# Kernel optimization log

Hardware: AMD Instinct MI355X
Metric: run time of the kernel (lower is better)

## Reference

```python
import math
import jax, jax.numpy as jnp
from jax import lax
import numpy as np

B, HH, WW = 8, 128, 128
N = HH * WW
DIM, NH = 256, 4
HD = DIM // 2 // NH          # 32, per-head dim of the halved channels
CH = DIM // 2                # 128
THETA, MAXSEQ = 10000.0, 4096

# --- static FoPE frequency setup (mirrors RotaryEmbedding.get_inv_freq with fope=True) ---
def _inv_freq():
    rot = 2 * HD                                   # rotary dim = d_model//n_heads = 2*head_dim
    inv = 1.0 / THETA ** (np.arange(0, rot, 2, dtype=np.float64) / rot)
    return inv[inv >= 2.0 * np.pi / MAXSEQ].astype(np.float32)

INV_FREQ = _inv_freq()
D_IN = int(INV_FREQ.shape[0])                      # 23
D_OUT = D_IN if D_IN <= (2 * HD) // 4 else (2 * HD) // 4   # 16


def _coef(key, gain=0.5):
    # xavier_normal_ on (NH, D_IN, D_OUT) + step-eye offset, as in FourierEmbedding.__init__
    fan_in, fan_out = D_IN * D_OUT, NH * D_OUT
    std = gain * math.sqrt(2.0 / (fan_in + fan_out))
    c = std * jax.random.normal(key, (NH, D_IN, D_OUT), jnp.float32)
    step = math.ceil(D_IN / D_OUT)
    eye = np.zeros((NH, D_IN, D_OUT), np.float32)
    for i in range(D_OUT):
        if i * step < D_IN:
            eye[:, i * step, i] = 1.0
    return c + jnp.asarray(eye)


def setup_inputs() -> dict:
    key = jax.random.key(0)
    ks = jax.random.split(key, 10)
    def lin(k, o, i):
        lim = 1.0 / math.sqrt(i)
        return jax.random.uniform(k, (o, i), jnp.float32, -lim, lim)
    return {
        "x": jax.random.normal(ks[0], (B, N, DIM), jnp.float32),
        "Wq": lin(ks[1], CH, DIM), "bq": jnp.zeros((CH,), jnp.float32),
        "Wk": lin(ks[2], CH, DIM), "bk": jnp.zeros((CH,), jnp.float32),
        "Wv": lin(ks[3], CH, DIM), "bv": jnp.zeros((CH,), jnp.float32),
        # Hedgehog maps init as identity
        "Whq": jnp.eye(HD, dtype=jnp.float32), "bhq": jnp.zeros((HD,), jnp.float32),
        "Whk": jnp.eye(HD, dtype=jnp.float32), "bhk": jnp.zeros((HD,), jnp.float32),
        "sin_coef": _coef(ks[4]), "cos_coef": _coef(ks[5]),
        "lepe_w": 0.02 * jax.random.normal(ks[6], (CH, 1, 3, 3), jnp.float32),
        "lepe_b": jnp.zeros((CH,), jnp.float32),
        "temperature": jnp.ones((CH, 1), jnp.float32),
        "Wp": lin(ks[7], DIM, DIM), "bp": jnp.zeros((DIM,), jnp.float32),
        "h": HH, "w": WW,
    }


def _hedgehog(t, W, b):
    # t: [b,h,n,HD] -> [b,h,n,2*HD]
    y = jnp.einsum('bhnd,ed->bhne', t, W) + b
    return jax.nn.softmax(jnp.concatenate([2.0 * y, -2.0 * y], axis=-1), axis=-1)


def _fope(t, sin_coef, cos_coef, n):
    # t: [b,h,n,2*HD]; learnable Fourier rotary
    freqs = jnp.arange(n, dtype=jnp.float32)[:, None] * jnp.asarray(INV_FREQ)[None, :]  # [n,D_IN]
    cs = sin_coef / sin_coef.sum(axis=-2, keepdims=True)
    cc = cos_coef / cos_coef.sum(axis=-2, keepdims=True)
    fs = jnp.einsum('tD,hDd->htd', jnp.sin(freqs), cs)[None]   # [1,h,n,D_OUT]
    fc = jnp.einsum('tD,hDd->htd', jnp.cos(freqs), cc)[None]
    pad = ((0, 0), (0, 0), (0, 0), (0, HD - D_OUT))
    fs = jnp.pad(fs, pad, constant_values=1.0)
    fc = jnp.pad(fc, pad, constant_values=1.0)
    fs = jnp.concatenate([fs, fs], axis=-1)                    # [1,h,n,2*HD]
    fc = jnp.concatenate([fc, fc], axis=-1)
    x1, x2 = t[..., :HD], t[..., HD:]
    rot = jnp.concatenate([-x2, x1], axis=-1)
    return t * fc - rot * fs


def _forward(x, Wq, bq, Wk, bk, Wv, bv, Whq, bhq, Whk, bhk,
             sin_coef, cos_coef, lepe_w, lepe_b, temperature, Wp, bp, h, w):
    b, n, _ = x.shape
    q = x @ Wq.T + bq   # [b,n,CH]
    k = x @ Wk.T + bk
    v = x @ Wv.T + bv

    # ---- spatial brand (Hedgehog linear attention with Fourier rotary) ----
    qh = q.reshape(b, n, NH, HD).swapaxes(1, 2)   # [b,nh,n,HD]
    kh = k.reshape(b, n, NH, HD).swapaxes(1, 2)
    vh = v.reshape(b, n, NH, HD).swapaxes(1, 2)
    qf = _hedgehog(qh, Whq, bhq)                  # [b,nh,n,2HD]
    kf = _hedgehog(kh, Whk, bhk)
    q_fope = _fope(qf, sin_coef, cos_coef, n)
    k_fope = _fope(kf, sin_coef, cos_coef, n)
    kmean = kf.mean(axis=-2, keepdims=True)                       # [b,nh,1,2HD]
    z = 1.0 / (jnp.einsum('bhnd,bhsd->bhns', qf, kmean) + 1e-6)   # [b,nh,n,1]
    s = n ** (-0.5)
    kv = jnp.einsum('bhnd,bhne->bhde', k_fope * s, vh * s)        # [b,nh,2HD,HD]
    xs = jnp.einsum('bhnd,bhde->bhne', q_fope, kv) * z            # [b,nh,n,HD]
    xs = xs.swapaxes(1, 2).reshape(b, n, CH)
    v_img = vh.swapaxes(-1, -2).reshape(b, CH, h, w)
    conv = lax.conv_general_dilated(v_img, lepe_w, (1, 1), 'SAME',
                                    feature_group_count=CH,
                                    dimension_numbers=('NCHW', 'OIHW', 'NCHW'))
    conv = conv + lepe_b[None, :, None, None]
    x_spatial = conv.reshape(b, CH, n).transpose(0, 2, 1) + xs    # [b,n,CH]

    # ---- channel brand (transposed attention over channels) ----
    qc = q.swapaxes(-1, -2)   # [b,CH,n]
    kc = k.swapaxes(-1, -2)
    vc = v.swapaxes(-1, -2)
    qn = qc / jnp.maximum(jnp.linalg.norm(qc, axis=-1, keepdims=True), 1e-12)
    kn = kc / jnp.maximum(jnp.linalg.norm(kc, axis=-1, keepdims=True), 1e-12)
    attn = jax.nn.softmax(jnp.einsum('bcl,bdl->bcd', qn, kn) * temperature, axis=-1)
    x_channel = jnp.einsum('bcd,bdl->bcl', attn, vc).swapaxes(-1, -2)  # [b,n,CH]

    out = jnp.concatenate([x_spatial, x_channel], axis=-1) @ Wp.T + bp  # [b,n,DIM]
    return out, q, k


def reference(x, Wq, bq, Wk, bk, Wv, bv, Whq, bhq, Whk, bhk,
              sin_coef, cos_coef, lepe_w, lepe_b, temperature, Wp, bp, h, w):
    return _forward(x, Wq, bq, Wk, bk, Wv, bv, Whq, bhq, Whk, bhk,
                    sin_coef, cos_coef, lepe_w, lepe_b, temperature, Wp, bp, h, w)
```

## Files before the change

kernel.cpp:

```cpp
#include <hip/hip_runtime.h>
#include <cmath>

#define NB 8
#define NN 16384
#define DIN 23
#define DOUT 16

typedef short bf16x8 __attribute__((ext_vector_type(8)));
typedef float f32x4 __attribute__((ext_vector_type(4)));

__device__ __forceinline__ unsigned short f2bf(float f) {
    unsigned int u = __float_as_uint(f);
    u += 0x7FFFu + ((u >> 16) & 1u);
    return (unsigned short)(u >> 16);
}
__device__ __forceinline__ float bf2f(unsigned short s) {
    return __uint_as_float(((unsigned int)s) << 16);
}
__device__ __forceinline__ float rcpf(float x) { return __builtin_amdgcn_rcpf(x); }

__device__ __forceinline__ bf16x8 cvt8(float4 a, float4 b) {
    bf16x8 r;
    r[0]=(short)f2bf(a.x); r[1]=(short)f2bf(a.y); r[2]=(short)f2bf(a.z); r[3]=(short)f2bf(a.w);
    r[4]=(short)f2bf(b.x); r[5]=(short)f2bf(b.y); r[6]=(short)f2bf(b.z); r[7]=(short)f2bf(b.w);
    return r;
}
__device__ __forceinline__ void red16(f32x4& s) {
    #pragma unroll
    for (int off = 1; off < 16; off <<= 1) {
        s[0] += __shfl_xor(s[0], off); s[1] += __shfl_xor(s[1], off);
        s[2] += __shfl_xor(s[2], off); s[3] += __shfl_xor(s[3], off);
    }
}
__device__ __forceinline__ void red16x2(f32x4& s, f32x4& w) {
    #pragma unroll
    for (int off = 1; off < 16; off <<= 1) {
        s[0] += __shfl_xor(s[0], off); s[1] += __shfl_xor(s[1], off);
        s[2] += __shfl_xor(s[2], off); s[3] += __shfl_xor(s[3], off);
        w[0] += __shfl_xor(w[0], off); w[1] += __shfl_xor(w[1], off);
        w[2] += __shfl_xor(w[2], off); w[3] += __shfl_xor(w[3], off);
    }
}

#define WS_XSPB   ((size_t)0)
#define WS_GPART  ((size_t)8388608)
#define WS_VB     ((size_t)16777216)
#define WS_XSB    ((size_t)25165824)
#define WS_FS     ((size_t)33554432)
#define WS_INV    ((size_t)35651584)
#define WS_CS     ((size_t)35651648)
#define WS_CC     ((size_t)35653184)
#define WS_WCAT   ((size_t)35654720)
#define WS_BCAT   ((size_t)35703872)
#define WS_KVPART ((size_t)35704256)
#define WS_KMPART ((size_t)37801408)
#define WS_KV     ((size_t)37866944)
#define WS_KMEAN  ((size_t)37932480)
#define WS_QN2    ((size_t)37934528)
#define WS_KN2    ((size_t)37935552)
#define WS_ATTN   ((size_t)38067648)
#define WS_BMATT  ((size_t)38198720)
#define WS_QB     ((size_t)38460864)
#define WS_KB     ((size_t)46849472)

__global__ void k_setup(const float* __restrict__ sc, const float* __restrict__ ccin,
                        float* __restrict__ inv, float* __restrict__ cs, float* __restrict__ cc)
{
    int t = threadIdx.x;
    if (t < DIN) inv[t] = (float)pow(10000.0, -((double)(2 * t)) / 64.0);
    int h = t >> 4, d = t & 15;
    float ss = 0.f, s2 = 0.f;
    for (int D = 0; D < DIN; ++D) { ss += sc[(h*DIN + D)*DOUT + d]; s2 += ccin[(h*DIN + D)*DOUT + d]; }
    float rs = 1.f / ss, r2 = 1.f / s2;
    for (int D = 0; D < DIN; ++D) {
        cs[(h*DIN + D)*DOUT + d] = sc[(h*DIN + D)*DOUT + d] * rs;
        cc[(h*DIN + D)*DOUT + d] = ccin[(h*DIN + D)*DOUT + d] * r2;
    }
}

__global__ __launch_bounds__(256) void k_tables(const float* __restrict__ inv, const float* __restrict__ cs,
                                                const float* __restrict__ cc,
                                                unsigned int* __restrict__ fsc)
{
    int t = threadIdx.x;
    int sub = t >> 6, lane = t & 63;
    int tpos = blockIdx.x*4 + sub;
    __shared__ float ssin[4][DIN], scos[4][DIN];
    if (lane < DIN) { float fr = (float)tpos * inv[lane]; ssin[sub][lane] = sinf(fr); scos[sub][lane] = cosf(fr); }
    __syncthreads();
    int h = lane >> 4, d = lane & 15;
    float as = 0.f, ac = 0.f;
    for (int D = 0; D < DIN; ++D) { as += ssin[sub][D]*cs[(h*DIN + D)*DOUT + d]; ac += scos[sub][D]*cc[(h*DIN + D)*DOUT + d]; }
    fsc[((size_t)h*NN + tpos)*16 + d] = ((unsigned int)f2bf(ac) << 16) | (unsigned int)f2bf(as);
}

__global__ __launch_bounds__(256) void k_wprep(
    const float* __restrict__ Wq, const float* __restrict__ Wk, const float* __restrict__ Wv,
    const float* __restrict__ bq, const float* __restrict__ bk, const float* __restrict__ bv,
    unsigned short* __restrict__ Wc, float* __restrict__ bcat)
{
    int row = blockIdx.x, t = threadIdx.x;
    const float* W = (row < 128) ? Wq : (row < 256) ? Wk : Wv;
    const float* bb = (row < 128) ? bq : (row < 256) ? bk : bv;
    int r = row & 127;
    Wc[(size_t)row*256 + t] = f2bf(W[(size_t)r*256 + t]);
    if (t == 0) bcat[row] = bb[r];
}

__global__ __launch_bounds__(256) void k_qkv_mfma(const float* __restrict__ x,
    const unsigned short* __restrict__ Wc, const float* __restrict__ bcat,
    float* __restrict__ q, float* __restrict__ k,
    unsigned short* __restrict__ qb, unsigned short* __restrict__ kb,
    unsigned short* __restrict__ vb)
{
    __shared__ unsigned short Asm[128*64];
    __shared__ unsigned short Bsm[128*64];
    int t = threadIdx.x;
    int lin = blockIdx.y*3 + blockIdx.x;
    int logical = (lin & 7)*384 + (lin >> 3);
    int ntile = logical % 3;
    int mtile = logical / 3;
    int m0 = mtile * 128;
    int n0 = ntile * 128;
    int wave = t >> 6, lane = t & 63;
    int wm = wave >> 1, wn = wave & 1;
    int lrow = lane & 15, lk = lane >> 4;
    f32x4 acc[4][4];
    #pragma unroll
    for (int i = 0; i < 4; ++i)
        #pragma unroll
        for (int j = 0; j < 4; ++j) acc[i][j] = (f32x4){0.f,0.f,0.f,0.f};

    int am = t >> 4, ak4 = t & 15;
    size_t arow = (size_t)(m0 + am);
    float4 pa[8];
    #pragma unroll
    for (int p = 0; p < 8; ++p)
        pa[p] = *reinterpret_cast<const float4*>(&x[(arow + p*16)*256 + ak4*4]);

    #pragma unroll
    for (int kt = 0; kt < 4; ++kt) {
        int k0 = kt * 64;
        if (kt) __syncthreads();
        #pragma unroll
        for (int p = 0; p < 8; ++p) {
            int m = am + p*16;
            ushort4 b4;
            b4.x = f2bf(pa[p].x); b4.y = f2bf(pa[p].y); b4.z = f2bf(pa[p].z); b4.w = f2bf(pa[p].w);
            int byte = m*128 + ((ak4*8) ^ ((m & 7) << 4));
            *reinterpret_cast<ushort4*>(reinterpret_cast<char*>(Asm) + byte) = b4;
        }
        {
            int n = t >> 3, k8 = t & 7;
            #pragma unroll
            for (int p = 0; p < 4; ++p, n += 32) {
                uint4 u4 = *reinterpret_cast<const uint4*>(&Wc[(size_t)(n0 + n)*256 + k0 + k8*8]);
                int byte = n*128 + ((k8 ^ (n & 7)) << 4);
                *reinterpret_cast<uint4*>(reinterpret_cast<char*>(Bsm) + byte) = u4;
            }
        }
        if (kt < 3) {
            #pragma unroll
            for (int p = 0; p < 8; ++p)
                pa[p] = *reinterpret_cast<const float4*>(&x[(arow + p*16)*256 + (kt+1)*64 + ak4*4]);
        }
        __syncthreads();
        #pragma unroll
        for (int ks = 0; ks < 2; ++ks) {
            bf16x8 af[4], bfv[4];
            #pragma unroll
            for (int mi = 0; mi < 4; ++mi) {
                int m = wm*64 + mi*16 + lrow;
                int u = (ks*4 + lk) ^ (m & 7);
                af[mi] = *reinterpret_cast<const bf16x8*>(reinterpret_cast<const char*>(Asm) + m*128 + u*16);
            }
            #pragma unroll
            for (int ni = 0; ni < 4; ++ni) {
                int n = wn*64 + ni*16 + lrow;
                int u = (ks*4 + lk) ^ (n & 7);
                bfv[ni] = *reinterpret_cast<const bf16x8*>(reinterpret_cast<const char*>(Bsm) + n*128 + u*16);
            }
            #pragma unroll
            for (int mi = 0; mi < 4; ++mi)
                #pragma unroll
                for (int ni = 0; ni < 4; ++ni)
                    acc[mi][ni] = __builtin_amdgcn_mfma_f32_16x16x32_bf16(af[mi], bfv[ni], acc[mi][ni], 0, 0, 0);
        }
    }
    #pragma unroll
    for (int mi = 0; mi < 4; ++mi) {
        #pragma unroll
        for (int ni = 0; ni < 4; ++ni) {
            int gcol = n0 + wn*64 + ni*16 + lrow;
            int c = gcol & 127;
            float bias = bcat[gcol];
            #pragma unroll
            for (int r = 0; r < 4; ++r) {
                size_t grow = (size_t)m0 + wm*64 + mi*16 + lk*4 + r;
                float val = acc[mi][ni][r] + bias;
                if (ntile == 0)      { q[grow*128 + c] = val; qb[grow*128 + c] = f2bf(val); }
                else if (ntile == 1) { k[grow*128 + c] = val; kb[grow*128 + c] = f2bf(val); }
                else                 vb[grow*128 + c] = f2bf(val);
            }
        }
    }
}

__global__ __launch_bounds__(256) void k_conv(const unsigned short* __restrict__ vb, const float* __restrict__ w,
                                              const float* __restrict__ bias, unsigned short* __restrict__ xspb)
{
    __shared__ float wsmT[9][128];
    __shared__ float bsm[128];
    int t = threadIdx.x;
    for (int i = t; i < 1152; i += 256) wsmT[i % 9][i / 9] = w[i];
    if (t < 128) bsm[t] = bias[t];
    __syncthreads();
    int jj = t >> 4, c8 = (t & 15) * 8;
    int j = blockIdx.x * 16 + jj;
    int i = blockIdx.y, b = blockIdx.z;
    float acc[8];
    #pragma unroll
    for (int l = 0; l < 8; ++l) acc[l] = bsm[c8 + l];
    #pragma unroll
    for (int di = 0; di < 3; ++di) {
        int ii = i + di - 1;
        if (ii < 0 || ii >= 128) continue;
        #pragma unroll
        for (int dj = 0; dj < 3; ++dj) {
            int jx = j + dj - 1;
            if (jx < 0 || jx >= 128) continue;
            uint4 u = *reinterpret_cast<const uint4*>(&vb[((size_t)b*NN + ii*128 + jx)*128 + c8]);
            const unsigned short* us = (const unsigned short*)&u;
            int kk = di*3 + dj;
            #pragma unroll
            for (int l = 0; l < 8; ++l)
                acc[l] += wsmT[kk][c8 + l] * bf2f(us[l]);
        }
    }
    ushort4 r0, r1;
    r0.x = f2bf(acc[0]); r0.y = f2bf(acc[1]); r0.z = f2bf(acc[2]); r0.w = f2bf(acc[3]);
    r1.x = f2bf(acc[4]); r1.y = f2bf(acc[5]); r1.z = f2bf(acc[6]); r1.w = f2bf(acc[7]);
    size_t ob = ((size_t)b*NN + i*128 + j)*128 + c8;
    *reinterpret_cast<ushort4*>(&xspb[ob]) = r0;
    *reinterpret_cast<ushort4*>(&xspb[ob+4]) = r1;
}

__global__ __launch_bounds__(256) void k_featkv(
    const unsigned short* __restrict__ kb, const unsigned short* __restrict__ vb,
    const float* __restrict__ W, const float* __restrict__ bvec,
    const unsigned int* __restrict__ fsc,
    float* __restrict__ kvpart, float* __restrict__ kmpart)
{
    __shared__ __align__(16) char smem[34816];
    __shared__ float kms[4][64];
    int bh = blockIdx.y, b = bh >> 2, h = bh & 3;
    int chunk = blockIdx.x;
    int t = threadIdx.x, w = t >> 6, lane = t & 63;
    int c = lane & 15, g = lane >> 4;
    unsigned short* kfsTw = reinterpret_cast<unsigned short*>(smem) + w*2560;
    unsigned short* vTw   = reinterpret_cast<unsigned short*>(smem + 20480) + w*1280;
    bf16x8 wb[2];
    #pragma unroll
    for (int et = 0; et < 2; ++et) {
        float4 wa = *reinterpret_cast<const float4*>(&W[(c + et*16)*32 + g*8]);
        float4 wb2 = *reinterpret_cast<const float4*>(&W[(c + et*16)*32 + g*8 + 4]);
        wb[et] = cvt8(wa, wb2);
    }
    float bias0 = bvec[c], bias1 = bvec[c + 16];
    f32x4 acc[4][2];
    #pragma unroll
    for (int i = 0; i < 4; ++i) { acc[i][0] = (f32x4){0.f,0.f,0.f,0.f}; acc[i][1] = (f32x4){0.f,0.f,0.f,0.f}; }
    f32x4 km0 = {0.f,0.f,0.f,0.f}, km1 = km0, km2 = km0, km3 = km0;

    for (int rnd = 0; rnd < 4; ++rnd) {
        int p0 = chunk*512 + w*128 + rnd*32;
        {
            uint4 vr0, vr1;
            size_t vbase = ((size_t)(b*NN + p0 + c*2))*128 + h*32 + g*8;
            vr0 = *reinterpret_cast<const uint4*>(&vb[vbase]);
            vr1 = *reinterpret_cast<const uint4*>(&vb[vbase + 128]);
            #pragma unroll
            for (int j = 0; j < 8; ++j) {
                ushort2 pk;
                pk.x = ((const unsigned short*)&vr0)[j];
                pk.y = ((const unsigned short*)&vr1)[j];
                *reinterpret_cast<ushort2*>(&vTw[(g*8 + j)*40 + c*2]) = pk;
            }
        }
        #pragma unroll
        for (int mt = 0; mt < 2; ++mt) {
            int posA = p0 + mt*16 + c;
            bf16x8 af = *reinterpret_cast<const bf16x8*>(&kb[((size_t)(b*NN + posA))*128 + h*32 + g*8]);
            f32x4 z4 = {0.f,0.f,0.f,0.f};
            f32x4 y0 = __builtin_amdgcn_mfma_f32_16x16x32_bf16(af, wb[0], z4, 0, 0, 0);
            f32x4 y1 = __builtin_amdgcn_mfma_f32_16x16x32_bf16(af, wb[1], z4, 0, 0, 0);
            f32x4 el0, eh0, el1, eh1;
            #pragma unroll
            for (int r = 0; r < 4; ++r) {
                float a0 = 2.f*(y0[r] + bias0);
                float a1 = 2.f*(y1[r] + bias1);
                el0[r] = __expf(a0); eh0[r] = __expf(-a0);
                el1[r] = __expf(a1); eh1[r] = __expf(-a1);
            }
            f32x4 s = el0 + eh0 + el1 + eh1;
            red16(s);
            f32x4 rs;
            #pragma unroll
            for (int r = 0; r < 4; ++r) rs[r] = rcpf(s[r]);
            f32x4 klo0 = el0*rs, khi0 = eh0*rs, klo1 = el1*rs, khi1 = eh1*rs;
            km0 += klo0; km1 += khi0; km2 += klo1; km3 += khi1;
            int posC = p0 + mt*16 + g*4;
            ushort4 wlo0, whi0, wlo1, whi1;
            #pragma unroll
            for (int r = 0; r < 4; ++r) {
                unsigned int u = fsc[((size_t)h*NN + posC + r)*16 + c];
                float fsv = bf2f((unsigned short)(u & 0xffffu));
                float fcv = bf2f((unsigned short)(u >> 16));
                ((unsigned short*)&wlo0)[r] = f2bf(klo0[r]*fcv + khi0[r]*fsv);
                ((unsigned short*)&whi0)[r] = f2bf(khi0[r]*fcv - klo0[r]*fsv);
                ((unsigned short*)&wlo1)[r] = f2bf(klo1[r] + khi1[r]);
                ((unsigned short*)&whi1)[r] = f2bf(khi1[r] - klo1[r]);
            }
            int po = mt*16 + g*4;
            *reinterpret_cast<ushort4*>(&kfsTw[(c)*40 + po])      = wlo0;
            *reinterpret_cast<ushort4*>(&kfsTw[(32 + c)*40 + po]) = whi0;
            *reinterpret_cast<ushort4*>(&kfsTw[(16 + c)*40 + po]) = wlo1;
            *reinterpret_cast<ushort4*>(&kfsTw[(48 + c)*40 + po]) = whi1;
        }
        {
            bf16x8 bf0 = *reinterpret_cast<const bf16x8*>(&vTw[(c)*40 + g*8]);
            bf16x8 bf1 = *reinterpret_cast<const bf16x8*>(&vTw[(16 + c)*40 + g*8]);
            #pragma unroll
            for (int mt = 0; mt < 4; ++mt) {
                bf16x8 af2 = *reinterpret_cast<const bf16x8*>(&kfsTw[(mt*16 + c)*40 + g*8]);
                acc[mt][0] = __builtin_amdgcn_mfma_f32_16x16x32_bf16(af2, bf0, acc[mt][0], 0, 0, 0);
                acc[mt][1] = __builtin_amdgcn_mfma_f32_16x16x32_bf16(af2, bf1, acc[mt][1], 0, 0, 0);
            }
        }
    }
    float kv0 = km0[0]+km0[1]+km0[2]+km0[3];
    float kv1 = km1[0]+km1[1]+km1[2]+km1[3];
    float kv2 = km2[0]+km2[1]+km2[2]+km2[3];
    float kv3 = km3[0]+km3[1]+km3[2]+km3[3];
    kv0 += __shfl_xor(kv0, 16); kv0 += __shfl_xor(kv0, 32);
    kv1 += __shfl_xor(kv1, 16); kv1 += __shfl_xor(kv1, 32);
    kv2 += __shfl_xor(kv2, 16); kv2 += __shfl_xor(kv2, 32);
    kv3 += __shfl_xor(kv3, 16); kv3 += __shfl_xor(kv3, 32);
    if (g == 0) {
        kms[w][c] = kv0; kms[w][16 + c] = kv2; kms[w][32 + c] = kv1; kms[w][48 + c] = kv3;
    }
    __syncthreads();
    float* kvred = reinterpret_cast<float*>(smem);
    #pragma unroll
    for (int mt = 0; mt < 4; ++mt)
        #pragma unroll
        for (int nt = 0; nt < 2; ++nt) {
            int d = nt*16 + c;
            *reinterpret_cast<f32x4*>(&kvred[(size_t)(w*32 + d)*68 + mt*16 + g*4]) = acc[mt][nt];
        }
    __syncthreads();
    #pragma unroll
    for (int i = 0; i < 8; ++i) {
        int idx = t*8 + i;
        int f = idx >> 5, d = idx & 31;
        float s2 = kvred[(0*32 + d)*68 + f] + kvred[(1*32 + d)*68 + f]
                 + kvred[(2*32 + d)*68 + f] + kvred[(3*32 + d)*68 + f];
        kvpart[((size_t)(bh*32 + chunk))*2048 + idx] = s2;
    }
    if (t < 64) {
        float s2 = kms[0][t] + kms[1][t] + kms[2][t] + kms[3][t];
        kmpart[(size_t)(bh*32 + chunk)*64 + t] = s2;
    }
}

__global__ __launch_bounds__(256) void k_kvred2(const float* __restrict__ kvpart, const float* __restrict__ kmpart,
                                                unsigned short* __restrict__ kvT, float* __restrict__ kmean)
{
    int bh = blockIdx.x >> 3, part = blockIdx.x & 7;
    int idx = part*256 + threadIdx.x;
    float s = 0.f;
    for (int cidx = 0; cidx < 32; ++cidx) s += kvpart[((size_t)(bh*32 + cidx))*2048 + idx];
    int f = idx >> 5, d = idx & 31;
    kvT[(size_t)bh*2048 + d*64 + f] = f2bf(s * (1.f/16384.f));
    if (part == 0 && threadIdx.x < 64) {
        int tt = threadIdx.x;
        float sm = 0.f;
        for (int cidx = 0; cidx < 32; ++cidx) sm += kmpart[(size_t)(bh*32 + cidx)*64 + tt];
        kmean[bh*64 + tt] = sm * (1.f/16384.f);
    }
}

__global__ __launch_bounds__(256) void k_featxs(
    const unsigned short* __restrict__ qb, const float* __restrict__ W, const float* __restrict__ bvec,
    const unsigned int* __restrict__ fsc, const unsigned short* __restrict__ kvT,
    const float* __restrict__ kmean, const unsigned short* __restrict__ xspb, unsigned short* __restrict__ xsb)
{
    __shared__ __align__(16) unsigned short qfs[4][32][72];
    int bh = blockIdx.y, b = bh >> 2, h = bh & 3;
    int chunk = blockIdx.x;
    int t = threadIdx.x, w = t >> 6, lane = t & 63;
    int c = lane & 15, g = lane >> 4;
    bf16x8 wb[2];
    #pragma unroll
    for (int et = 0; et < 2; ++et) {
        float4 wa = *reinterpret_cast<const float4*>(&W[(c + et*16)*32 + g*8]);
        float4 wb2 = *reinterpret_cast<const float4*>(&W[(c + et*16)*32 + g*8 + 4]);
        wb[et] = cvt8(wa, wb2);
    }
    float bias0 = bvec[c], bias1 = bvec[c + 16];
    float kml0 = kmean[bh*64 + c],      kml1 = kmean[bh*64 + 16 + c];
    float kmh0 = kmean[bh*64 + 32 + c], kmh1 = kmean[bh*64 + 48 + c];
    bf16x8 bkv[2][2];
    #pragma unroll
    for (int nt = 0; nt < 2; ++nt)
        #pragma unroll
        for (int ks = 0; ks < 2; ++ks)
            bkv[nt][ks] = *reinterpret_cast<const bf16x8*>(&kvT[(size_t)bh*2048 + (nt*16 + c)*64 + ks*32 + g*8]);

    for (int rnd = 0; rnd < 4; ++rnd) {
        int p0 = chunk*512 + w*128 + rnd*32;
        #pragma unroll
        for (int mt = 0; mt < 2; ++mt) {
            int posA = p0 + mt*16 + c;
            bf16x8 af = *reinterpret_cast<const bf16x8*>(&qb[((size_t)(b*NN + posA))*128 + h*32 + g*8]);
            f32x4 z4 = {0.f,0.f,0.f,0.f};
            f32x4 y0 = __builtin_amdgcn_mfma_f32_16x16x32_bf16(af, wb[0], z4, 0, 0, 0);
            f32x4 y1 = __builtin_amdgcn_mfma_f32_16x16x32_bf16(af, wb[1], z4, 0, 0, 0);
            f32x4 el0, eh0, el1, eh1;
            #pragma unroll
            for (int r = 0; r < 4; ++r) {
                float a0 = 2.f*(y0[r] + bias0);
                float a1 = 2.f*(y1[r] + bias1);
                el0[r] = __expf(a0); eh0[r] = __expf(-a0);
                el1[r] = __expf(a1); eh1[r] = __expf(-a1);
            }
            f32x4 s = el0 + eh0 + el1 + eh1;
            f32x4 wv = el0*kml0 + eh0*kmh0 + el1*kml1 + eh1*kmh1;
            red16x2(s, wv);
            f32x4 zr;
            #pragma unroll
            for (int r = 0; r < 4; ++r) {
                float rs = rcpf(s[r]);
                float z = rcpf(wv[r]*rs + 1e-6f);
                zr[r] = z*rs;
            }
            int posC = mt*16 + g*4;
            #pragma unroll
            for (int r = 0; r < 4; ++r) {
                unsigned int u = fsc[((size_t)h*NN + p0 + posC + r)*16 + c];
                float fsv = bf2f((unsigned short)(u & 0xffffu));
                float fcv = bf2f((unsigned short)(u >> 16));
                qfs[w][posC + r][c]      = f2bf(zr[r]*(el0[r]*fcv + eh0[r]*fsv));
                qfs[w][posC + r][32 + c] = f2bf(zr[r]*(eh0[r]*fcv - el0[r]*fsv));
                qfs[w][posC + r][16 + c] = f2bf(zr[r]*(el1[r] + eh1[r]));
                qfs[w][posC + r][48 + c] = f2bf(zr[r]*(eh1[r] - el1[r]));
            }
        }
        f32x4 acc[2][2];
        #pragma unroll
        for (int i = 0; i < 2; ++i) { acc[i][0] = (f32x4){0.f,0.f,0.f,0.f}; acc[i][1] = (f32x4){0.f,0.f,0.f,0.f}; }
        #pragma unroll
        for (int ks = 0; ks < 2; ++ks)
            #pragma unroll
            for (int mt = 0; mt < 2; ++mt) {
                bf16x8 af2 = *reinterpret_cast<const bf16x8*>(&qfs[w][mt*16 + c][ks*32 + g*8]);
                acc[mt][0] = __builtin_amdgcn_mfma_f32_16x16x32_bf16(af2, bkv[0][ks], acc[mt][0], 0, 0, 0);
                acc[mt][1] = __builtin_amdgcn_mfma_f32_16x16x32_bf16(af2, bkv[1][ks], acc[mt][1], 0, 0, 0);
            }
        #pragma unroll
        for (int mt = 0; mt < 2; ++mt)
            #pragma unroll
            for (int nt = 0; nt < 2; ++nt) {
                int d = nt*16 + c;
                #pragma unroll
                for (int r = 0; r < 4; ++r) {
                    int pos = p0 + mt*16 + g*4 + r;
                    size_t off = ((size_t)(b*NN + pos))*128 + h*32 + d;
                    xsb[off] = f2bf(bf2f(xspb[off]) + acc[mt][nt][r]);
                }
            }
    }
}

__global__ __launch_bounds__(256) void k_gram(const unsigned short* __restrict__ qb, const unsigned short* __restrict__ kb,
                                              float* __restrict__ Gpart,
                                              float* __restrict__ qn2, float* __restrict__ kn2)
{
    __shared__ unsigned short qTs[128][40];
    __shared__ unsigned short kTs[128][40];
    int kc = blockIdx.x, bb = blockIdx.y;
    int t = threadIdx.x, lane = t & 63;
    int wave = t >> 6, wm = wave >> 1, wn = wave & 1;
    int c = t & 127, lh = t >> 7;
    float qa = 0.f, ka = 0.f;
    f32x4 acc[4][4];
    #pragma unroll
    for (int i = 0; i < 4; ++i)
        #pragma unroll
        for (int j = 0; j < 4; ++j) acc[i][j] = (f32x4){0.f,0.f,0.f,0.f};

    for (int kt = 0; kt < 8; ++kt) {
        __syncthreads();
        #pragma unroll
        for (int i = 0; i < 16; ++i) {
            int l = lh*16 + i;
            size_t pos = (size_t)bb*NN + kc*256 + kt*32 + l;
            unsigned short qu = qb[pos*128 + c];
            unsigned short ku = kb[pos*128 + c];
            float qv = bf2f(qu), kvv = bf2f(ku);
            qa += qv*qv; ka += kvv*kvv;
            qTs[c][l] = qu;
            kTs[c][l] = ku;
        }
        __syncthreads();
        bf16x8 af[4];
        #pragma unroll
        for (int mi = 0; mi < 4; ++mi)
            af[mi] = *reinterpret_cast<const bf16x8*>(&qTs[wm*64 + mi*16 + (lane & 15)][(lane >> 4)*8]);
        #pragma unroll
        for (int ni = 0; ni < 4; ++ni) {
            bf16x8 bfr = *reinterpret_cast<const bf16x8*>(&kTs[wn*64 + ni*16 + (lane & 15)][(lane >> 4)*8]);
            #pragma unroll
            for (int mi = 0; mi < 4; ++mi)
                acc[mi][ni] = __builtin_amdgcn_mfma_f32_16x16x32_bf16(af[mi], bfr, acc[mi][ni], 0, 0, 0);
        }
    }
    size_t gb = ((size_t)(bb*64 + kc))*16384;
    #pragma unroll
    for (int mi = 0; mi < 4; ++mi) {
        #pragma unroll
        for (int ni = 0; ni < 4; ++ni) {
            int d = wn*64 + ni*16 + (lane & 15);
            #pragma unroll
            for (int r = 0; r < 4; ++r) {
                int cc = wm*64 + mi*16 + (lane >> 4)*4 + r;
                Gpart[gb + (size_t)cc*128 + d] = acc[mi][ni][r];
            }
        }
    }
    atomicAdd(&qn2[bb*128 + c], qa);
    atomicAdd(&kn2[bb*128 + c], ka);
}

__global__ __launch_bounds__(128) void k_attnsm(const float* __restrict__ Gpart, const float* __restrict__ qn2,
    const float* __restrict__ kn2, const float* __restrict__ temp, float* __restrict__ attn)
{
    __shared__ float red[128];
    int row = blockIdx.x;
    int b = row >> 7, c = row & 127;
    int t = threadIdx.x;
    float s0 = 0.f;
    for (int kc = 0; kc < 64; ++kc)
        s0 += Gpart[((size_t)(b*64 + kc))*16384 + (size_t)c*128 + t];
    float qn = fmaxf(sqrtf(qn2[b*128 + c]), 1e-12f);
    float kn = fmaxf(sqrtf(kn2[b*128 + t]), 1e-12f);
    float val = s0 / (qn*kn) * temp[c];
    red[t] = val; __syncthreads();
    for (int s = 64; s > 0; s >>= 1) { if (t < s) red[t] = fmaxf(red[t], red[t+s]); __syncthreads(); }
    float mm = red[0]; __syncthreads();
    float ev = expf(val - mm);
    red[t] = ev; __syncthreads();
    for (int s = 64; s > 0; s >>= 1) { if (t < s) red[t] += red[t+s]; __syncthreads(); }
    attn[(size_t)row*128 + t] = ev / red[0];
}

__global__ __launch_bounds__(256) void k_bmat(const float* __restrict__ attn, const float* __restrict__ Wp,
                                              unsigned short* __restrict__ BmatT)
{
    int b = blockIdx.y, kk = blockIdx.x, o = threadIdx.x;
    float val;
    if (kk < 128) {
        val = Wp[(size_t)o*256 + kk];
    } else {
        int d = kk - 128;
        __shared__ float a[128];
        if (o < 128) a[o] = attn[((size_t)b*128 + o)*128 + d];
        __syncthreads();
        float acc = 0.f;
        for (int c = 0; c < 128; ++c) acc += a[c] * Wp[(size_t)o*256 + 128 + c];
        val = acc;
    }
    BmatT[((size_t)b*256 + o)*256 + kk] = f2bf(val);
}

__global__ __launch_bounds__(256) void k_out_mfma(const unsigned short* __restrict__ xsb,
    const unsigned short* __restrict__ vb, const unsigned short* __restrict__ BmatT,
    const float* __restrict__ bp, float* __restrict__ out)
{
    __shared__ unsigned short Asm[128*64];
    __shared__ unsigned short Bsm[128*64];
    int t = threadIdx.x;
    int lin = blockIdx.y*2 + blockIdx.x;
    int logical = (lin & 7)*256 + (lin >> 3);
    int ntile = logical & 1;
    int mtile = logical >> 1;
    int m0 = mtile * 128;
    int n0 = ntile * 128;
    int b = mtile >> 7;
    int wave = t >> 6, lane = t & 63;
    int wm = wave >> 1, wn = wave & 1;
    int lrow = lane & 15, lk = lane >> 4;
    f32x4 acc[4][4];
    #pragma unroll
    for (int i = 0; i < 4; ++i)
        #pragma unroll
        for (int j = 0; j < 4; ++j) acc[i][j] = (f32x4){0.f,0.f,0.f,0.f};

    int am = t >> 3, ak8 = t & 7;
    uint4 pa4[4];
    #pragma unroll
    for (int p = 0; p < 4; ++p)
        pa4[p] = *reinterpret_cast<const uint4*>(&xsb[(size_t)(m0 + am + p*32)*128 + ak8*8]);

    #pragma unroll
    for (int kt = 0; kt < 4; ++kt) {
        if (kt) __syncthreads();
        #pragma unroll
        for (int p = 0; p < 4; ++p) {
            int m = am + p*32;
            int byte = m*128 + ((ak8 ^ (m & 7)) << 4);
            *reinterpret_cast<uint4*>(reinterpret_cast<char*>(Asm) + byte) = pa4[p];
        }
        {
            int n = t >> 3, k8 = t & 7;
            #pragma unroll
            for (int p = 0; p < 4; ++p, n += 32) {
                uint4 u4 = *reinterpret_cast<const uint4*>(&BmatT[((size_t)b*256 + n0 + n)*256 + kt*64 + k8*8]);
                int byte = n*128 + ((k8 ^ (n & 7)) << 4);
                *reinterpret_cast<uint4*>(reinterpret_cast<char*>(Bsm) + byte) = u4;
            }
        }
        if (kt < 3) {
            const unsigned short* Asrc = ((kt+1) < 2) ? xsb : vb;
            int ka0 = ((kt+1) & 1) * 64;
            #pragma unroll
            for (int p = 0; p < 4; ++p)
                pa4[p] = *reinterpret_cast<const uint4*>(&Asrc[(size_t)(m0 + am + p*32)*128 + ka0 + ak8*8]);
        }
        __syncthreads();
        #pragma unroll
        for (int ks = 0; ks < 2; ++ks) {
            bf16x8 af[4], bfv[4];
            #pragma unroll
            for (int mi = 0; mi < 4; ++mi) {
                int m = wm*64 + mi*16 + lrow;
                int u = (ks*4 + lk) ^ (m & 7);
                af[mi] = *reinterpret_cast<const bf16x8*>(reinterpret_cast<const char*>(Asm) + m*128 + u*16);
            }
            #pragma unroll
            for (int ni = 0; ni < 4; ++ni) {
                int n = wn*64 + ni*16 + lrow;
                int u = (ks*4 + lk) ^ (n & 7);
                bfv[ni] = *reinterpret_cast<const bf16x8*>(reinterpret_cast<const char*>(Bsm) + n*128 + u*16);
            }
            #pragma unroll
            for (int mi = 0; mi < 4; ++mi)
                #pragma unroll
                for (int ni = 0; ni < 4; ++ni)
                    acc[mi][ni] = __builtin_amdgcn_mfma_f32_16x16x32_bf16(af[mi], bfv[ni], acc[mi][ni], 0, 0, 0);
        }
    }
    #pragma unroll
    for (int mi = 0; mi < 4; ++mi) {
        #pragma unroll
        for (int ni = 0; ni < 4; ++ni) {
            int gcol = n0 + wn*64 + ni*16 + lrow;
            float bias = bp[gcol];
            #pragma unroll
            for (int r = 0; r < 4; ++r) {
                size_t grow = (size_t)m0 + wm*64 + mi*16 + lk*4 + r;
                out[grow*256 + gcol] = acc[mi][ni][r] + bias;
            }
        }
    }
}

extern "C" void kernel_launch(void* const* d_in, const int* in_sizes, int n_in,
                              void* d_out, int out_size, void* d_ws, size_t ws_size,
                              hipStream_t stream)
{
    (void)in_sizes; (void)n_in; (void)out_size; (void)ws_size;
    const float* x    = (const float*)d_in[0];
    const float* Wq   = (const float*)d_in[1];
    const float* bq   = (const float*)d_in[2];
    const float* Wk   = (const float*)d_in[3];
    const float* bk   = (const float*)d_in[4];
    const float* Wv   = (const float*)d_in[5];
    const float* bv   = (const float*)d_in[6];
    const float* Whq  = (const float*)d_in[7];
    const float* bhq  = (const float*)d_in[8];
    const float* Whk  = (const float*)d_in[9];
    const float* bhk  = (const float*)d_in[10];
    const float* sinc = (const float*)d_in[11];
    const float* cosc = (const float*)d_in[12];
    const float* lw   = (const float*)d_in[13];
    const float* lb   = (const float*)d_in[14];
    const float* temp = (const float*)d_in[15];
    const float* Wp   = (const float*)d_in[16];
    const float* bp   = (const float*)d_in[17];

    float* out = (float*)d_out;
    float* q   = out + 33554432;
    float* k   = out + 50331648;
    float* ws  = (float*)d_ws;

    unsigned short* xspb = (unsigned short*)(ws + WS_XSPB);
    float* Gpart  = ws + WS_GPART;
    unsigned short* vbuf = (unsigned short*)(ws + WS_VB);
    unsigned short* xsb  = (unsigned short*)(ws + WS_XSB);
    unsigned int* fsc = (unsigned int*)(ws + WS_FS);
    float* inv    = ws + WS_INV;
    float* cs     = ws + WS_CS;
    float* cc     = ws + WS_CC;
    unsigned short* Wc = (unsigned short*)(ws + WS_WCAT);
    float* bcat   = ws + WS_BCAT;
    float* kvpart = ws + WS_KVPART;
    float* kmpart = ws + WS_KMPART;
    unsigned short* kvT = (unsigned short*)(ws + WS_KV);
    float* kmean  = ws + WS_KMEAN;
    float* qn2    = ws + WS_QN2;
    float* kn2    = ws + WS_KN2;
    float* attn   = ws + WS_ATTN;
    unsigned short* BmatT = (unsigned short*)(ws + WS_BMATT);
    unsigned short* qbuf  = (unsigned short*)(ws + WS_QB);
    unsigned short* kbuf  = (unsigned short*)(ws + WS_KB);

    hipMemsetAsync(qn2, 0, 2048*sizeof(float), stream);

    k_setup<<<1, 64, 0, stream>>>(sinc, cosc, inv, cs, cc);
    k_tables<<<4096, 256, 0, stream>>>(inv, cs, cc, fsc);
    k_wprep<<<384, 256, 0, stream>>>(Wq, Wk, Wv, bq, bk, bv, Wc, bcat);
    k_qkv_mfma<<<dim3(3, 1024), 256, 0, stream>>>(x, Wc, bcat, q, k, qbuf, kbuf, vbuf);
    k_conv<<<dim3(8, 128, 8), 256, 0, stream>>>(vbuf, lw, lb, xspb);
    k_featkv<<<dim3(32, 32), 256, 0, stream>>>(kbuf, vbuf, Whk, bhk, fsc, kvpart, kmpart);
    k_kvred2<<<256, 256, 0, stream>>>(kvpart, kmpart, kvT, kmean);
    k_featxs<<<dim3(32, 32), 256, 0, stream>>>(qbuf, Whq, bhq, fsc, kvT, kmean, xspb, xsb);
    k_gram<<<dim3(64, 8), 256, 0, stream>>>(qbuf, kbuf, Gpart, qn2, kn2);
    k_attnsm<<<1024, 128, 0, stream>>>(Gpart, qn2, kn2, temp, attn);
    k_bmat<<<dim3(256, 8), 256, 0, stream>>>(attn, Wp, BmatT);
    k_out_mfma<<<dim3(2, 1024), 256, 0, stream>>>(xsb, vbuf, BmatT, bp, out);
}
```

Before: 384.8 us.

## Compute full QKV row tile per block and merge setup into weight-prep kernel

The QKV projection kernel now has each 512-thread block compute all 384 output columns for a 128-row tile, instead of three separate 128-column blocks. Each x tile is therefore loaded from global memory and converted to bf16 once rather than three times. The cost is more registers per thread (a 4x6 accumulator grid) and 64KB of shared memory per block, which may lower occupancy. Separately, the small setup kernel is folded into the weight-prep kernel as one extra block, saving a kernel launch.

```diff
diff --git a/kernel.cpp b/kernel.cpp
--- a/kernel.cpp
+++ b/kernel.cpp
@@ -63,19 +63,32 @@
 #define WS_QB     ((size_t)38460864)
 #define WS_KB     ((size_t)46849472)
 
-__global__ void k_setup(const float* __restrict__ sc, const float* __restrict__ ccin,
-                        float* __restrict__ inv, float* __restrict__ cs, float* __restrict__ cc)
-{
-    int t = threadIdx.x;
-    if (t < DIN) inv[t] = (float)pow(10000.0, -((double)(2 * t)) / 64.0);
-    int h = t >> 4, d = t & 15;
-    float ss = 0.f, s2 = 0.f;
-    for (int D = 0; D < DIN; ++D) { ss += sc[(h*DIN + D)*DOUT + d]; s2 += ccin[(h*DIN + D)*DOUT + d]; }
-    float rs = 1.f / ss, r2 = 1.f / s2;
-    for (int D = 0; D < DIN; ++D) {
-        cs[(h*DIN + D)*DOUT + d] = sc[(h*DIN + D)*DOUT + d] * rs;
-        cc[(h*DIN + D)*DOUT + d] = ccin[(h*DIN + D)*DOUT + d] * r2;
-    }
+__global__ __launch_bounds__(256) void k_wprep(
+    const float* __restrict__ Wq, const float* __restrict__ Wk, const float* __restrict__ Wv,
+    const float* __restrict__ bq, const float* __restrict__ bk, const float* __restrict__ bv,
+    const float* __restrict__ sc, const float* __restrict__ ccin,
+    unsigned short* __restrict__ Wc, float* __restrict__ bcat,
+    float* __restrict__ inv, float* __restrict__ cs, float* __restrict__ cc)
+{
+    int row = blockIdx.x, t = threadIdx.x;
+    if (row == 384) {
+        if (t >= 64) return;
+        if (t < DIN) inv[t] = (float)pow(10000.0, -((double)(2 * t)) / 64.0);
+        int h = t >> 4, d = t & 15;
+        float ss = 0.f, s2 = 0.f;
+        for (int D = 0; D < DIN; ++D) { ss += sc[(h*DIN + D)*DOUT + d]; s2 += ccin[(h*DIN + D)*DOUT + d]; }
+        float rs = 1.f / ss, r2 = 1.f / s2;
+        for (int D = 0; D < DIN; ++D) {
+            cs[(h*DIN + D)*DOUT + d] = sc[(h*DIN + D)*DOUT + d] * rs;
+            cc[(h*DIN + D)*DOUT + d] = ccin[(h*DIN + D)*DOUT + d] * r2;
+        }
+        return;
+    }
+    const float* W = (row < 128) ? Wq : (row < 256) ? Wk : Wv;
+    const float* bb = (row < 128) ? bq : (row < 256) ? bk : bv;
+    int r = row & 127;
+    Wc[(size_t)row*256 + t] = f2bf(W[(size_t)r*256 + t]);
+    if (t == 0) bcat[row] = bb[r];
 }
 
 __global__ __launch_bounds__(256) void k_tables(const float* __restrict__ inv, const float* __restrict__ cs,
@@ -94,112 +107,93 @@
     fsc[((size_t)h*NN + tpos)*16 + d] = ((unsigned int)f2bf(ac) << 16) | (unsigned int)f2bf(as);
 }
 
-__global__ __launch_bounds__(256) void k_wprep(
-    const float* __restrict__ Wq, const float* __restrict__ Wk, const float* __restrict__ Wv,
-    const float* __restrict__ bq, const float* __restrict__ bk, const float* __restrict__ bv,
-    unsigned short* __restrict__ Wc, float* __restrict__ bcat)
-{
-    int row = blockIdx.x, t = threadIdx.x;
-    const float* W = (row < 128) ? Wq : (row < 256) ? Wk : Wv;
-    const float* bb = (row < 128) ? bq : (row < 256) ? bk : bv;
-    int r = row & 127;
-    Wc[(size_t)row*256 + t] = f2bf(W[(size_t)r*256 + t]);
-    if (t == 0) bcat[row] = bb[r];
-}
-
-__global__ __launch_bounds__(256) void k_qkv_mfma(const float* __restrict__ x,
+__global__ __launch_bounds__(512) void k_qkv_mfma(const float* __restrict__ x,
     const unsigned short* __restrict__ Wc, const float* __restrict__ bcat,
     float* __restrict__ q, float* __restrict__ k,
     unsigned short* __restrict__ qb, unsigned short* __restrict__ kb,
     unsigned short* __restrict__ vb)
 {
-    __shared__ unsigned short Asm[128*64];
-    __shared__ unsigned short Bsm[128*64];
+    __shared__ __align__(16) char smem[65536];
     int t = threadIdx.x;
-    int lin = blockIdx.y*3 + blockIdx.x;
-    int logical = (lin & 7)*384 + (lin >> 3);
-    int ntile = logical % 3;
-    int mtile = logical / 3;
+    int lin = blockIdx.x;
+    int mtile = (lin & 7)*128 + (lin >> 3);
     int m0 = mtile * 128;
-    int n0 = ntile * 128;
     int wave = t >> 6, lane = t & 63;
-    int wm = wave >> 1, wn = wave & 1;
+    int wm = wave >> 2, wn = wave & 3;
     int lrow = lane & 15, lk = lane >> 4;
-    f32x4 acc[4][4];
+    f32x4 acc[4][6];
     #pragma unroll
     for (int i = 0; i < 4; ++i)
         #pragma unroll
-        for (int j = 0; j < 4; ++j) acc[i][j] = (f32x4){0.f,0.f,0.f,0.f};
+        for (int j = 0; j < 6; ++j) acc[i][j] = (f32x4){0.f,0.f,0.f,0.f};
 
     int am = t >> 4, ak4 = t & 15;
     size_t arow = (size_t)(m0 + am);
-    float4 pa[8];
-    #pragma unroll
-    for (int p = 0; p < 8; ++p)
-        pa[p] = *reinterpret_cast<const float4*>(&x[(arow + p*16)*256 + ak4*4]);
+    float4 pa[4];
+    #pragma unroll
+    for (int p = 0; p < 4; ++p)
+        pa[p] = *reinterpret_cast<const float4*>(&x[(arow + p*32)*256 + ak4*4]);
 
     #pragma unroll
     for (int kt = 0; kt < 4; ++kt) {
         int k0 = kt * 64;
         if (kt) __syncthreads();
         #pragma unroll
-        for (int p = 0; p < 8; ++p) {
-            int m = am + p*16;
+        for (int p = 0; p < 4; ++p) {
+            int m = am + p*32;
             ushort4 b4;
             b4.x = f2bf(pa[p].x); b4.y = f2bf(pa[p].y); b4.z = f2bf(pa[p].z); b4.w = f2bf(pa[p].w);
             int byte = m*128 + ((ak4*8) ^ ((m & 7) << 4));
-            *reinterpret_cast<ushort4*>(reinterpret_cast<char*>(Asm) + byte) = b4;
+            *reinterpret_cast<ushort4*>(smem + byte) = b4;
         }
         {
             int n = t >> 3, k8 = t & 7;
             #pragma unroll
-            for (int p = 0; p < 4; ++p, n += 32) {
-                uint4 u4 = *reinterpret_cast<const uint4*>(&Wc[(size_t)(n0 + n)*256 + k0 + k8*8]);
+            for (int p = 0; p < 6; ++p, n += 64) {
+                uint4 u4 = *reinterpret_cast<const uint4*>(&Wc[(size_t)n*256 + k0 + k8*8]);
                 int byte = n*128 + ((k8 ^ (n & 7)) << 4);
-                *reinterpret_cast<uint4*>(reinterpret_cast<char*>(Bsm) + byte) = u4;
+                *reinterpret_cast<uint4*>(smem + 16384 + byte) = u4;
             }
         }
         if (kt < 3) {
             #pragma unroll
-            for (int p = 0; p < 8; ++p)
-                pa[p] = *reinterpret_cast<const float4*>(&x[(arow + p*16)*256 + (kt+1)*64 + ak4*4]);
+            for (int p = 0; p < 4; ++p)
+                pa[p] = *reinterpret_cast<const float4*>(&x[(arow + p*32)*256 + (kt+1)*64 + ak4*4]);
         }
         __syncthreads();
         #pragma unroll
         for (int ks = 0; ks < 2; ++ks) {
-            bf16x8 af[4], bfv[4];
+            bf16x8 af[4];
             #pragma unroll
             for (int mi = 0; mi < 4; ++mi) {
                 int m = wm*64 + mi*16 + lrow;
                 int u = (ks*4 + lk) ^ (m & 7);
-                af[mi] = *reinterpret_cast<const bf16x8*>(reinterpret_cast<const char*>(Asm) + m*128 + u*16);
-            }
-            #pragma unroll
-            for (int ni = 0; ni < 4; ++ni) {
-                int n = wn*64 + ni*16 + lrow;
+                af[mi] = *reinterpret_cast<const bf16x8*>(smem + m*128 + u*16);
+            }
+            #pragma unroll
+            for (int ni = 0; ni < 6; ++ni) {
+                int n = wn*96 + ni*16 + lrow;
                 int u = (ks*4 + lk) ^ (n & 7);
-                bfv[ni] = *reinterpret_cast<const bf16x8*>(reinterpret_cast<const char*>(Bsm) + n*128 + u*16);
-            }
-            #pragma unroll
-            for (int mi = 0; mi < 4; ++mi)
+                bf16x8 bfv = *reinterpret_cast<const bf16x8*>(smem + 16384 + n*128 + u*16);
                 #pragma unroll
-                for (int ni = 0; ni < 4; ++ni)
-                    acc[mi][ni] = __builtin_amdgcn_mfma_f32_16x16x32_bf16(af[mi], bfv[ni], acc[mi][ni], 0, 0, 0);
+                for (int mi = 0; mi < 4; ++mi)
+                    acc[mi][ni] = __builtin_amdgcn_mfma_f32_16x16x32_bf16(af[mi], bfv, acc[mi][ni], 0, 0, 0);
+            }
         }
     }
     #pragma unroll
     for (int mi = 0; mi < 4; ++mi) {
         #pragma unroll
-        for (int ni = 0; ni < 4; ++ni) {
-            int gcol = n0 + wn*64 + ni*16 + lrow;
+        for (int ni = 0; ni < 6; ++ni) {
+            int gcol = wn*96 + ni*16 + lrow;
             int c = gcol & 127;
             float bias = bcat[gcol];
             #pragma unroll
             for (int r = 0; r < 4; ++r) {
                 size_t grow = (size_t)m0 + wm*64 + mi*16 + lk*4 + r;
                 float val = acc[mi][ni][r] + bias;
-                if (ntile == 0)      { q[grow*128 + c] = val; qb[grow*128 + c] = f2bf(val); }
-                else if (ntile == 1) { k[grow*128 + c] = val; kb[grow*128 + c] = f2bf(val); }
+                if (gcol < 128)      { q[grow*128 + c] = val; qb[grow*128 + c] = f2bf(val); }
+                else if (gcol < 256) { k[grow*128 + c] = val; kb[grow*128 + c] = f2bf(val); }
                 else                 vb[grow*128 + c] = f2bf(val);
             }
         }
@@ -727,10 +721,9 @@
 
     hipMemsetAsync(qn2, 0, 2048*sizeof(float), stream);
 
-    k_setup<<<1, 64, 0, stream>>>(sinc, cosc, inv, cs, cc);
+    k_wprep<<<385, 256, 0, stream>>>(Wq, Wk, Wv, bq, bk, bv, sinc, cosc, Wc, bcat, inv, cs, cc);
     k_tables<<<4096, 256, 0, stream>>>(inv, cs, cc, fsc);
-    k_wprep<<<384, 256, 0, stream>>>(Wq, Wk, Wv, bq, bk, bv, Wc, bcat);
-    k_qkv_mfma<<<dim3(3, 1024), 256, 0, stream>>>(x, Wc, bcat, q, k, qbuf, kbuf, vbuf);
+    k_qkv_mfma<<<1024, 512, 0, stream>>>(x, Wc, bcat, q, k, qbuf, kbuf, vbuf);
     k_conv<<<dim3(8, 128, 8), 256, 0, stream>>>(vbuf, lw, lb, xspb);
     k_featkv<<<dim3(32, 32), 256, 0, stream>>>(kbuf, vbuf, Whk, bhk, fsc, kvpart, kmpart);
     k_kvred2<<<256, 256, 0, stream>>>(kvpart, kmpart, kvT, kmean);
```

New measurement: 367.5 us. -4.5%, faster.
